# Kernel tuning notes

Hardware: AMD Instinct MI355X
Metric: run time of the kernel (lower is better)

The kernel has to match this reference:

```python
import jax, jax.numpy as jnp
import numpy as np

DIM = 2048          # args.dim
E = 16              # n_routed_experts
TOPK = 2            # n_activated_experts
H = 1408            # moe_inter_dim (expert hidden)
N_SHARED = 2        # n_shared_experts
HS = H * N_SHARED   # shared expert hidden
B, S = 2, 2048
TEMP = 1.0          # gate_temperature


def setup_inputs() -> dict:
    key = jax.random.key(0)
    ks = jax.random.split(key, 8)
    sc = 0.02
    return {
        "x": jax.random.normal(ks[0], (B, S, DIM), dtype=jnp.float32),
        "gate_w": jax.random.normal(ks[1], (E, DIM), dtype=jnp.float32) * sc,
        "w1": jax.random.normal(ks[2], (E, H, DIM), dtype=jnp.float32) * sc,
        "w2": jax.random.normal(ks[3], (E, DIM, H), dtype=jnp.float32) * sc,
        "w3": jax.random.normal(ks[4], (E, H, DIM), dtype=jnp.float32) * sc,
        "sw1": jax.random.normal(ks[5], (HS, DIM), dtype=jnp.float32) * sc,
        "sw2": jax.random.normal(ks[6], (DIM, HS), dtype=jnp.float32) * sc,
        "sw3": jax.random.normal(ks[7], (HS, DIM), dtype=jnp.float32) * sc,
    }


def reference(x, gate_w, w1, w2, w3, sw1, sw2, sw3):
    b, s, d = x.shape
    xf = x.reshape(-1, d)  # [T, D]

    # shared expert (SwiGLU FFN)
    sh = jax.nn.silu(xf @ sw1.T) * (xf @ sw3.T)      # [T, HS]
    shared_out = sh @ sw2.T                           # [T, D]

    # gate (eval mode: no input noise)
    scores = (xf @ gate_w.T) / TEMP                   # [T, E]
    probs = jax.nn.softmax(scores, axis=-1)
    topk_vals, topk_idx = jax.lax.top_k(probs, TOPK)  # sorted desc, matches torch.topk
    topk_vals = topk_vals / (topk_vals.sum(-1, keepdims=True) + 1e-9)

    # combine weights per (token, expert); zero where expert not selected
    w = (jax.nn.one_hot(topk_idx, E, dtype=xf.dtype) * topk_vals[..., None]).sum(1)  # [T, E]

    # all-expert SwiGLU, weighted-combined (w==0 exactly zeroes unselected experts)
    h1 = jnp.einsum('td,ehd->teh', xf, w1)            # [T, E, H]
    h3 = jnp.einsum('td,ehd->teh', xf, w3)
    act = jax.nn.silu(h1) * h3 * w[:, :, None]
    y = jnp.einsum('teh,edh->td', act, w2) + shared_out

    # aux load-balancing loss
    importance = probs.mean(0)                        # [E]
    load = w.sum(0) / (w.sum() + 1e-9)                # [E]
    aux_loss = E * (importance * load).sum()

    return y.reshape(b, s, d), aux_loss
```

## Files before the change

### kernel.cpp

```cpp
#include <hip/hip_runtime.h>
#include <cstdint>

#define TOKS 4096
#define DIMD 2048
#define NE   16
#define HE   1408
#define HSH  2816
#define SLOTS 8192
#define SLOTP 8320
#define MAXTILES 128

typedef unsigned short u16;
typedef __attribute__((ext_vector_type(8))) __bf16 bf16x8;
typedef __attribute__((ext_vector_type(4))) float  f32x4;

__device__ inline unsigned f2bf_pack(float a, float b) {
  unsigned ua = __builtin_bit_cast(unsigned, a);
  unsigned ub = __builtin_bit_cast(unsigned, b);
  ua = (ua + 0x7FFFu + ((ua >> 16) & 1u)) >> 16;
  ub = (ub + 0x7FFFu + ((ub >> 16) & 1u)) >> 16;
  return ua | (ub << 16);
}
__device__ inline u16 f2bf(float a) {
  unsigned ua = __builtin_bit_cast(unsigned, a);
  return (u16)((ua + 0x7FFFu + ((ua >> 16) & 1u)) >> 16);
}
__device__ inline float bf2f(u16 u) {
  return __builtin_bit_cast(float, (unsigned)u << 16);
}
__device__ inline void gload_lds16(const u16* g, u16* l) {
  __builtin_amdgcn_global_load_lds((const __attribute__((address_space(1))) void*)g,
                                   (__attribute__((address_space(3))) void*)l, 16, 0, 0);
}

__global__ __launch_bounds__(64)
void gate2_kernel(const float* __restrict__ x, const float* __restrict__ gw,
                  float* __restrict__ probs, int* __restrict__ sel0, int* __restrict__ sel1,
                  float* __restrict__ wt0, float* __restrict__ wt1)
{
  const int t = blockIdx.x;
  const int l = threadIdx.x;
  const float4* xr = (const float4*)(x + (size_t)t * DIMD);
  float4 xv[8];
#pragma unroll
  for (int j = 0; j < 8; ++j) xv[j] = xr[j * 64 + l];

  float sc[16];
#pragma unroll
  for (int e = 0; e < 16; ++e) {
    const float4* g = (const float4*)(gw + (size_t)e * DIMD);
    float s = 0.f;
#pragma unroll
    for (int j = 0; j < 8; ++j) {
      float4 gv = g[j * 64 + l];
      s += xv[j].x * gv.x + xv[j].y * gv.y + xv[j].z * gv.z + xv[j].w * gv.w;
    }
#pragma unroll
    for (int o = 32; o > 0; o >>= 1) s += __shfl_down(s, o);
    sc[e] = s;
  }
  if (l == 0) {
    float mx = sc[0];
#pragma unroll
    for (int e = 1; e < 16; ++e) mx = fmaxf(mx, sc[e]);
    float pe[16]; float sum = 0.f;
#pragma unroll
    for (int e = 0; e < 16; ++e) { pe[e] = __expf(sc[e] - mx); sum += pe[e]; }
    float inv = 1.f / sum;
    int b0 = -1, b1 = -1; float v0 = -1.f, v1 = -1.f;
#pragma unroll
    for (int e = 0; e < 16; ++e) {
      float p = pe[e] * inv;
      probs[t * 16 + e] = p;
      if (p > v0) { v1 = v0; b1 = b0; v0 = p; b0 = e; }
      else if (p > v1) { v1 = p; b1 = e; }
    }
    float wsum = v0 + v1 + 1e-9f;
    sel0[t] = b0; sel1[t] = b1;
    wt0[t] = v0 / wsum; wt1[t] = v1 / wsum;
  }
}

__global__ __launch_bounds__(256)
void expert_count(const int* __restrict__ sel0, const int* __restrict__ sel1,
                  const float* __restrict__ wt0, const float* __restrict__ wt1,
                  int* __restrict__ counts, float* __restrict__ loadsum)
{
  const int e = blockIdx.x, tid = threadIdx.x;
  int c = 0; float s = 0.f;
  for (int t = tid; t < TOKS; t += 256) {
    if (sel0[t] == e) { c++; s += wt0[t]; }
    else if (sel1[t] == e) { c++; s += wt1[t]; }
  }
  __shared__ int ci[256]; __shared__ float sf[256];
  ci[tid] = c; sf[tid] = s; __syncthreads();
  for (int d = 128; d > 0; d >>= 1) {
    if (tid < d) { ci[tid] += ci[tid + d]; sf[tid] += sf[tid + d]; }
    __syncthreads();
  }
  if (tid == 0) { counts[e] = ci[0]; loadsum[e] = sf[0]; }
}

__global__ __launch_bounds__(256)
void offsets_aux(const float* __restrict__ probs, const int* __restrict__ counts,
                 const float* __restrict__ loadsum, int* __restrict__ offs,
                 int* __restrict__ tile_e, int* __restrict__ tile_m, int* __restrict__ meta,
                 float* __restrict__ out_aux)
{
  const int tid = threadIdx.x;
  float imp[16];
#pragma unroll
  for (int e = 0; e < 16; ++e) imp[e] = 0.f;
  for (int t = tid; t < TOKS; t += 256)
#pragma unroll
    for (int e = 0; e < 16; ++e) imp[e] += probs[t * 16 + e];

  __shared__ float red[256];
  __shared__ float impE[16];
  for (int e = 0; e < 16; ++e) {
    red[tid] = imp[e]; __syncthreads();
    for (int d = 128; d > 0; d >>= 1) {
      if (tid < d) red[tid] += red[tid + d];
      __syncthreads();
    }
    if (tid == 0) impE[e] = red[0];
    __syncthreads();
  }
  if (tid == 0) {
    int off = 0;
    for (int e = 0; e < 16; ++e) { offs[e] = off; off += counts[e]; }
    float tot = 0.f;
    for (int e = 0; e < 16; ++e) tot += loadsum[e];
    float aux = 0.f;
    for (int e = 0; e < 16; ++e) aux += (impE[e] / (float)TOKS) * (loadsum[e] / (tot + 1e-9f));
    *out_aux = 16.f * aux;
    int tile = 0;
    for (int e = 0; e < 16; ++e) {
      int nt = (counts[e] + 127) >> 7;
      for (int k = 0; k < nt; ++k) { tile_e[tile] = e; tile_m[tile] = k << 7; ++tile; }
    }
    meta[0] = tile;
  }
}

__global__ __launch_bounds__(256)
void rank_scatter(const int* __restrict__ sel0, const int* __restrict__ sel1,
                  const float* __restrict__ wt0, const float* __restrict__ wt1,
                  const int* __restrict__ offs, int* __restrict__ toklist2,
                  float* __restrict__ slotwt, int* __restrict__ tokslot)
{
  const int e = blockIdx.x, tid = threadIdx.x;
  const int t0 = tid * 16;
  unsigned flags = 0; int cloc = 0;
#pragma unroll
  for (int j = 0; j < 16; ++j) {
    int t = t0 + j;
    bool f = (sel0[t] == e) || (sel1[t] == e);
    flags |= ((unsigned)f) << j;
    cloc += f;
  }
  __shared__ int psum[256];
  psum[tid] = cloc; __syncthreads();
  for (int d = 1; d < 256; d <<= 1) {
    int v = (tid >= d) ? psum[tid - d] : 0;
    __syncthreads();
    psum[tid] += v;
    __syncthreads();
  }
  int r = offs[e] + psum[tid] - cloc;
  for (int j = 0; j < 16; ++j) {
    if ((flags >> j) & 1u) {
      int t = t0 + j;
      bool first = (sel0[t] == e);
      toklist2[r] = t;
      slotwt[r] = first ? wt0[t] : wt1[t];
      tokslot[2 * t + (first ? 0 : 1)] = r;
      r++;
    }
  }
}

__global__ __launch_bounds__(256)
void cvt_f32_bf16(const float4* __restrict__ src, uint2* __restrict__ dst, int n4)
{
  int i = blockIdx.x * 256 + threadIdx.x;
  int stride = gridDim.x * 256;
  for (; i < n4; i += stride) {
    float4 v = src[i];
    uint2 p; p.x = f2bf_pack(v.x, v.y); p.y = f2bf_pack(v.z, v.w);
    dst[i] = p;
  }
}

__global__ __launch_bounds__(256)
void cvt_expert(const float4* __restrict__ src, uint2* __restrict__ dst,
                int per_e4, int dstride4, int doff4, int total4)
{
  int i = blockIdx.x * 256 + threadIdx.x;
  int stride = gridDim.x * 256;
  for (; i < total4; i += stride) {
    int e = i / per_e4;
    int r = i - e * per_e4;
    float4 v = src[i];
    uint2 p; p.x = f2bf_pack(v.x, v.y); p.y = f2bf_pack(v.z, v.w);
    dst[(size_t)e * dstride4 + doff4 + r] = p;
  }
}

__global__ __launch_bounds__(256)
void gather2(const float* __restrict__ x, const int* __restrict__ toklist2,
             u16* __restrict__ Xg)
{
  int slot = blockIdx.x * 4 + (threadIdx.x >> 6);
  int l = threadIdx.x & 63;
  int tok = toklist2[slot];
  const float4* srcr = (const float4*)(x + (size_t)tok * DIMD);
  uint2* dstr = (uint2*)(Xg + (size_t)slot * DIMD);
#pragma unroll
  for (int j = 0; j < 8; ++j) {
    float4 v = srcr[j * 64 + l];
    uint2 q; q.x = f2bf_pack(v.x, v.y); q.y = f2bf_pack(v.z, v.w);
    dstr[j * 64 + l] = q;
  }
}

template<int MODE>
__global__ __launch_bounds__(256, 3)
void gemm128(const u16* __restrict__ A, const u16* __restrict__ Bg,
             u16* __restrict__ Obf, float* __restrict__ Of,
             const int* __restrict__ counts, const int* __restrict__ offs,
             const int* __restrict__ tile_e, const int* __restrict__ tile_m,
             const int* __restrict__ meta)
{
  constexpr int KD = (MODE == 0) ? DIMD : (MODE == 1) ? HSH : (MODE == 2) ? DIMD : HE;
  constexpr int ND = (MODE == 0) ? 2 * HSH : (MODE == 1) ? DIMD : (MODE == 2) ? HSH : DIMD;

  __shared__ u16 sA[128 * 64];
  __shared__ u16 sB[128 * 64];

  const int tid  = threadIdx.x;
  const int lane = tid & 63;
  const int wave = tid >> 6;
  const int wm = wave >> 1, wn = wave & 1;

  int mbase, nbase;
  int e = 0, cnt = 0, arow0;
  const u16* B = Bg;
  if constexpr (MODE >= 2) {
    int tix = blockIdx.y;
    if (tix >= meta[0]) return;
    e = tile_e[tix];
    cnt = counts[e];
    mbase = tile_m[tix];
    arow0 = offs[e] + mbase;
    nbase = blockIdx.x * 128;
    B = Bg + (size_t)e * ND * KD;
  } else {
    const int nx = gridDim.x;
    int bid = blockIdx.y * nx + blockIdx.x;
    int cpx = (nx * gridDim.y) >> 3;
    int swz = (bid & 7) * cpx + (bid >> 3);
    mbase = (swz / nx) * 128;
    nbase = (swz % nx) * 128;
    arow0 = mbase;
  }

  f32x4 acc[4][4];
#pragma unroll
  for (int i = 0; i < 4; ++i)
#pragma unroll
    for (int j = 0; j < 4; ++j) acc[i][j] = (f32x4){0.f, 0.f, 0.f, 0.f};

  const int srow  = lane >> 3;
  const int sslot = (lane & 7) ^ srow;
  const int scol  = sslot * 8;

  const u16* Bbase = B + (size_t)nbase * KD;

  for (int kb = 0; kb < KD; kb += 64) {
#pragma unroll
    for (int i = 0; i < 4; ++i) {
      int c = wave * 4 + i;
      int row = c * 8 + srow;
      size_t ar;
      if constexpr (MODE >= 2) {
        int rg = arow0 + row;
        if (rg > SLOTS - 1) rg = SLOTS - 1;
        ar = (size_t)rg * KD;
      } else {
        ar = (size_t)(arow0 + row) * KD;
      }
      gload_lds16(A + ar + kb + scol, &sA[c * 512]);
      gload_lds16(Bbase + (size_t)row * KD + kb + scol, &sB[c * 512]);
    }
    __syncthreads();

#pragma unroll
    for (int ks = 0; ks < 2; ++ks) {
      bf16x8 a[4], b[4];
#pragma unroll
      for (int mi = 0; mi < 4; ++mi) {
        int r = wm * 64 + mi * 16 + (lane & 15);
        int s = (ks * 4 + (lane >> 4)) ^ (r & 7);
        a[mi] = *(const bf16x8*)((const char*)sA + r * 128 + s * 16);
      }
#pragma unroll
      for (int ni = 0; ni < 4; ++ni) {
        int r = wn * 64 + ni * 16 + (lane & 15);
        int s = (ks * 4 + (lane >> 4)) ^ (r & 7);
        b[ni] = *(const bf16x8*)((const char*)sB + r * 128 + s * 16);
      }
#pragma unroll
      for (int mi = 0; mi < 4; ++mi)
#pragma unroll
        for (int ni = 0; ni < 4; ++ni)
          acc[mi][ni] = __builtin_amdgcn_mfma_f32_16x16x32_bf16(a[mi], b[ni], acc[mi][ni], 0, 0, 0);
    }
    __syncthreads();
  }

  const int lr4 = (lane >> 4) * 4;
  const int lc  = lane & 15;
#pragma unroll
  for (int mi = 0; mi < 4; ++mi) {
#pragma unroll
    for (int ni = 0; ni < 4; ++ni) {
#pragma unroll
      for (int r = 0; r < 4; ++r) {
        int lrow = wm * 64 + mi * 16 + lr4 + r;
        int col  = nbase + wn * 64 + ni * 16 + lc;
        float v = acc[mi][ni][r];
        if constexpr (MODE == 0) {
          Obf[(size_t)(mbase + lrow) * ND + col] = f2bf(v);
        } else if constexpr (MODE == 1) {
          Of[(size_t)(mbase + lrow) * ND + col] = v;
        } else {
          int grow = mbase + lrow;
          if (grow < cnt) Obf[(size_t)(arow0 + lrow) * ND + col] = f2bf(v);
        }
      }
    }
  }
}

__global__ __launch_bounds__(256)
void combine_sh(const u16* __restrict__ H, u16* __restrict__ U)
{
  int i = blockIdx.x * 256 + threadIdx.x;
  if (i >= TOKS * (HSH / 8)) return;
  int t = i / (HSH / 8);
  int c = (i - t * (HSH / 8)) * 8;
  const u16* h1p = H + (size_t)t * (2 * HSH) + c;
  uint4 va = *(const uint4*)h1p;
  uint4 vb = *(const uint4*)(h1p + HSH);
  const u16* ap = (const u16*)&va;
  const u16* bp = (const u16*)&vb;
  u16 o[8];
#pragma unroll
  for (int j = 0; j < 8; ++j) {
    float v1 = bf2f(ap[j]), v3 = bf2f(bp[j]);
    o[j] = f2bf((v1 / (1.f + __expf(-v1))) * v3);
  }
  *(uint4*)(U + (size_t)t * HSH + c) = *(const uint4*)o;
}

__global__ __launch_bounds__(256)
void combine_r(const u16* __restrict__ H, const float* __restrict__ slotwt,
               u16* __restrict__ Act)
{
  int i = blockIdx.x * 256 + threadIdx.x;
  if (i >= SLOTS * (HE / 8)) return;
  int t = i / (HE / 8);
  int c = (i - t * (HE / 8)) * 8;
  float wt = slotwt[t];
  const u16* h1p = H + (size_t)t * HSH + c;
  uint4 va = *(const uint4*)h1p;
  uint4 vb = *(const uint4*)(h1p + HE);
  const u16* ap = (const u16*)&va;
  const u16* bp = (const u16*)&vb;
  u16 o[8];
#pragma unroll
  for (int j = 0; j < 8; ++j) {
    float v1 = bf2f(ap[j]), v3 = bf2f(bp[j]);
    o[j] = f2bf((v1 / (1.f + __expf(-v1))) * v3 * wt);
  }
  *(uint4*)(Act + (size_t)t * HE + c) = *(const uint4*)o;
}

__global__ __launch_bounds__(256)
void finalize(const u16* __restrict__ Yslot, const int* __restrict__ tokslot,
              float* __restrict__ out)
{
  int i = blockIdx.x * 256 + threadIdx.x;
  int t = i >> 8;
  int c = (i & 255) * 8;
  int s0 = tokslot[2 * t], s1 = tokslot[2 * t + 1];
  uint4 a = *(const uint4*)(Yslot + (size_t)s0 * DIMD + c);
  uint4 b = *(const uint4*)(Yslot + (size_t)s1 * DIMD + c);
  const u16* ap = (const u16*)&a;
  const u16* bp = (const u16*)&b;
  float* op = out + (size_t)t * DIMD + c;
  float4 v0 = *(float4*)op, v1 = *(float4*)(op + 4);
  float vv[8] = {v0.x, v0.y, v0.z, v0.w, v1.x, v1.y, v1.z, v1.w};
#pragma unroll
  for (int j = 0; j < 8; ++j) vv[j] += bf2f(ap[j]) + bf2f(bp[j]);
  *(float4*)op = (float4){vv[0], vv[1], vv[2], vv[3]};
  *(float4*)(op + 4) = (float4){vv[4], vv[5], vv[6], vv[7]};
}

extern "C" void kernel_launch(void* const* d_in, const int* in_sizes, int n_in,
                              void* d_out, int out_size, void* d_ws, size_t ws_size,
                              hipStream_t stream) {
  const float* x      = (const float*)d_in[0];
  const float* gate_w = (const float*)d_in[1];
  const float* w1     = (const float*)d_in[2];
  const float* w2     = (const float*)d_in[3];
  const float* w3     = (const float*)d_in[4];
  const float* sw1    = (const float*)d_in[5];
  const float* sw2    = (const float*)d_in[6];
  const float* sw3    = (const float*)d_in[7];
  float* out = (float*)d_out;

  char* ws = (char*)d_ws;
  size_t o = 0;
  int*   counts   = (int*)(ws + o);   o += 256;
  int*   offsv    = (int*)(ws + o);   o += 256;
  float* loadsum  = (float*)(ws + o); o += 256;
  int*   tile_e   = (int*)(ws + o);   o += MAXTILES * 4;
  int*   tile_m   = (int*)(ws + o);   o += MAXTILES * 4;
  int*   meta     = (int*)(ws + o);   o += 256;
  int*   sel0     = (int*)(ws + o);   o += TOKS * 4;
  int*   sel1     = (int*)(ws + o);   o += TOKS * 4;
  float* wt0      = (float*)(ws + o); o += TOKS * 4;
  float* wt1      = (float*)(ws + o); o += TOKS * 4;
  int*   tokslot  = (int*)(ws + o);   o += TOKS * 2 * 4;
  int*   toklist2 = (int*)(ws + o);   o += SLOTS * 4;
  float* slotwt   = (float*)(ws + o); o += SLOTS * 4;
  float* probs    = (float*)(ws + o); o += TOKS * 16 * 4;

  o = 1 << 20;
  u16* xbf   = (u16*)(ws + o); o += (size_t)TOKS * DIMD * 2;
  u16* Xg    = (u16*)(ws + o); o += (size_t)SLOTP * DIMD * 2;
  u16* w13b  = (u16*)(ws + o); o += (size_t)NE * HSH * DIMD * 2;
  u16* w2b   = (u16*)(ws + o); o += (size_t)NE * DIMD * HE * 2;
  u16* sw13b = (u16*)(ws + o); o += (size_t)(2 * HSH) * DIMD * 2;
  u16* sw2b  = (u16*)(ws + o); o += (size_t)DIMD * HSH * 2;
  u16* H     = (u16*)(ws + o); o += (size_t)SLOTP * HSH * 2;
  u16* UA    = (u16*)(ws + o); o += (size_t)SLOTP * HE * 2;
  u16* Yslot = Xg;

  gate2_kernel<<<TOKS, 64, 0, stream>>>(x, gate_w, probs, sel0, sel1, wt0, wt1);
  expert_count<<<NE, 256, 0, stream>>>(sel0, sel1, wt0, wt1, counts, loadsum);
  offsets_aux<<<1, 256, 0, stream>>>(probs, counts, loadsum, offsv, tile_e, tile_m, meta,
                                     out + (size_t)TOKS * DIMD);
  rank_scatter<<<NE, 256, 0, stream>>>(sel0, sel1, wt0, wt1, offsv, toklist2, slotwt, tokslot);

  cvt_f32_bf16<<<2048, 256, 0, stream>>>((const float4*)x, (uint2*)xbf, TOKS * DIMD / 4);
  cvt_f32_bf16<<<1024, 256, 0, stream>>>((const float4*)sw1, (uint2*)sw13b, HSH * DIMD / 4);
  cvt_f32_bf16<<<1024, 256, 0, stream>>>((const float4*)sw3, (uint2*)sw13b + HSH * DIMD / 4, HSH * DIMD / 4);
  cvt_f32_bf16<<<1024, 256, 0, stream>>>((const float4*)sw2, (uint2*)sw2b, DIMD * HSH / 4);
  cvt_f32_bf16<<<4096, 256, 0, stream>>>((const float4*)w2, (uint2*)w2b, NE * DIMD * HE / 4);
  cvt_expert<<<4096, 256, 0, stream>>>((const float4*)w1, (uint2*)w13b,
                                       HE * DIMD / 4, HSH * DIMD / 4, 0, NE * HE * DIMD / 4);
  cvt_expert<<<4096, 256, 0, stream>>>((const float4*)w3, (uint2*)w13b,
                                       HE * DIMD / 4, HSH * DIMD / 4, HE * DIMD / 4, NE * HE * DIMD / 4);
  gather2<<<SLOTS / 4, 256, 0, stream>>>(x, toklist2, Xg);

  gemm128<0><<<dim3(2 * HSH / 128, TOKS / 128), 256, 0, stream>>>(
      xbf, sw13b, H, nullptr, nullptr, nullptr, nullptr, nullptr, nullptr);
  combine_sh<<<TOKS * (HSH / 8) / 256, 256, 0, stream>>>(H, UA);
  gemm128<1><<<dim3(DIMD / 128, TOKS / 128), 256, 0, stream>>>(
      UA, sw2b, nullptr, out, nullptr, nullptr, nullptr, nullptr, nullptr);

  gemm128<2><<<dim3(HSH / 128, 80), 256, 0, stream>>>(
      Xg, w13b, H, nullptr, counts, offsv, tile_e, tile_m, meta);
  combine_r<<<SLOTS * (HE / 8) / 256, 256, 0, stream>>>(H, slotwt, UA);
  gemm128<3><<<dim3(DIMD / 128, 80), 256, 0, stream>>>(
      UA, w2b, Yslot, nullptr, counts, offsv, tile_e, tile_m, meta);
  finalize<<<TOKS * DIMD / 8 / 256, 256, 0, stream>>>(Yslot, tokslot, out);
}
```

Measured before the change: 770.2 us.

## Use 256-wide double-buffered GEMM tiles with 512 threads and XCD-aware swizzle

```diff
diff --git a/kernel.cpp b/kernel.cpp
--- a/kernel.cpp
+++ b/kernel.cpp
@@ -136,8 +136,8 @@
     *out_aux = 16.f * aux;
     int tile = 0;
     for (int e = 0; e < 16; ++e) {
-      int nt = (counts[e] + 127) >> 7;
-      for (int k = 0; k < nt; ++k) { tile_e[tile] = e; tile_m[tile] = k << 7; ++tile; }
+      int nt = (counts[e] + 255) >> 8;
+      for (int k = 0; k < nt; ++k) { tile_e[tile] = e; tile_m[tile] = k << 8; ++tile; }
     }
     meta[0] = tile;
   }
@@ -224,9 +224,9 @@
   }
 }
 
-template<int MODE>
-__global__ __launch_bounds__(256, 3)
-void gemm128(const u16* __restrict__ A, const u16* __restrict__ Bg,
+template<int MODE, int BMT>
+__global__ __launch_bounds__(512, 2)
+void gemm256(const u16* __restrict__ A, const u16* __restrict__ Bg,
              u16* __restrict__ Obf, float* __restrict__ Of,
              const int* __restrict__ counts, const int* __restrict__ offs,
              const int* __restrict__ tile_e, const int* __restrict__ tile_m,
@@ -234,14 +234,17 @@
 {
   constexpr int KD = (MODE == 0) ? DIMD : (MODE == 1) ? HSH : (MODE == 2) ? DIMD : HE;
   constexpr int ND = (MODE == 0) ? 2 * HSH : (MODE == 1) ? DIMD : (MODE == 2) ? HSH : DIMD;
-
-  __shared__ u16 sA[128 * 64];
-  __shared__ u16 sB[128 * 64];
+  constexpr int BM = BMT * 32;
+  constexpr int NT = KD / 64;
+
+  __shared__ u16 sA[2][BM * 64];
+  __shared__ u16 sB[2][256 * 64];
 
   const int tid  = threadIdx.x;
   const int lane = tid & 63;
   const int wave = tid >> 6;
-  const int wm = wave >> 1, wn = wave & 1;
+  const int wm = wave >> 2;
+  const int wn = wave & 3;
 
   int mbase, nbase;
   int e = 0, cnt = 0, arow0;
@@ -253,82 +256,114 @@
     cnt = counts[e];
     mbase = tile_m[tix];
     arow0 = offs[e] + mbase;
-    nbase = blockIdx.x * 128;
+    nbase = blockIdx.x * 256;
     B = Bg + (size_t)e * ND * KD;
   } else {
     const int nx = gridDim.x;
+    int nwg = nx * gridDim.y;
     int bid = blockIdx.y * nx + blockIdx.x;
-    int cpx = (nx * gridDim.y) >> 3;
-    int swz = (bid & 7) * cpx + (bid >> 3);
-    mbase = (swz / nx) * 128;
-    nbase = (swz % nx) * 128;
+    int q = nwg >> 3, r2 = nwg & 7;
+    int xcd = bid & 7, pos = bid >> 3;
+    int wgid = (xcd < r2 ? xcd * (q + 1) : r2 * (q + 1) + (xcd - r2) * q) + pos;
+    mbase = (wgid / nx) * BM;
+    nbase = (wgid % nx) * 256;
     arow0 = mbase;
   }
 
-  f32x4 acc[4][4];
-#pragma unroll
-  for (int i = 0; i < 4; ++i)
+  f32x4 acc[BMT][4];
+#pragma unroll
+  for (int i = 0; i < BMT; ++i)
 #pragma unroll
     for (int j = 0; j < 4; ++j) acc[i][j] = (f32x4){0.f, 0.f, 0.f, 0.f};
 
-  const int srow  = lane >> 3;
-  const int sslot = (lane & 7) ^ srow;
-  const int scol  = sslot * 8;
-
+  const int srow = lane >> 3;
+  const int scol = ((lane & 7) ^ srow) * 8;
   const u16* Bbase = B + (size_t)nbase * KD;
 
-  for (int kb = 0; kb < KD; kb += 64) {
-#pragma unroll
-    for (int i = 0; i < 4; ++i) {
-      int c = wave * 4 + i;
-      int row = c * 8 + srow;
-      size_t ar;
-      if constexpr (MODE >= 2) {
-        int rg = arow0 + row;
-        if (rg > SLOTS - 1) rg = SLOTS - 1;
-        ar = (size_t)rg * KD;
-      } else {
-        ar = (size_t)(arow0 + row) * KD;
+  const u16* Asrc[BMT / 2];
+#pragma unroll
+  for (int i = 0; i < BMT / 2; ++i) {
+    int c = wave * (BMT / 2) + i;
+    int row = c * 8 + srow;
+    int rg = arow0 + row;
+    if constexpr (MODE >= 2) { if (rg > SLOTS - 1) rg = SLOTS - 1; }
+    Asrc[i] = A + (size_t)rg * KD + scol;
+  }
+  const u16* Bsrc[4];
+#pragma unroll
+  for (int i = 0; i < 4; ++i) {
+    int c = wave * 4 + i;
+    Bsrc[i] = Bbase + (size_t)(c * 8 + srow) * KD + scol;
+  }
+
+#define STAGE_T(bb, kb) do {                                                    \
+    _Pragma("unroll") for (int i_ = 0; i_ < BMT / 2; ++i_)                      \
+      gload_lds16(Asrc[i_] + (kb), &sA[bb][(wave * (BMT / 2) + i_) * 512]);     \
+    _Pragma("unroll") for (int i_ = 0; i_ < 4; ++i_)                            \
+      gload_lds16(Bsrc[i_] + (kb), &sB[bb][(wave * 4 + i_) * 512]);             \
+  } while (0)
+
+  const int lm = lane & 15, hi = lane >> 4;
+  int aoff0[BMT], boff0[4];
+#pragma unroll
+  for (int mi = 0; mi < BMT; ++mi) {
+    int r = wm * (BMT * 16) + mi * 16 + lm;
+    aoff0[mi] = r * 128 + ((hi ^ (r & 7)) << 4);
+  }
+#pragma unroll
+  for (int ni = 0; ni < 4; ++ni) {
+    int r = wn * 64 + ni * 16 + lm;
+    boff0[ni] = r * 128 + ((hi ^ (r & 7)) << 4);
+  }
+
+  STAGE_T(0, 0);
+  STAGE_T(1, 64);
+  int cur = 0;
+  for (int t = 0; t < NT; ++t) {
+    if (t < NT - 1) {
+      if constexpr (BMT == 8) asm volatile("s_waitcnt vmcnt(8)" ::: "memory");
+      else                    asm volatile("s_waitcnt vmcnt(6)" ::: "memory");
+    } else {
+      asm volatile("s_waitcnt vmcnt(0)" ::: "memory");
+    }
+    __builtin_amdgcn_s_barrier();
+    __builtin_amdgcn_sched_barrier(0);
+
+    const char* sAc = (const char*)&sA[cur][0];
+    const char* sBc = (const char*)&sB[cur][0];
+    __builtin_amdgcn_s_setprio(1);
+#pragma unroll
+    for (int ks = 0; ks < 2; ++ks) {
+      const int kx = ks << 6;
+      bf16x8 b[4];
+#pragma unroll
+      for (int ni = 0; ni < 4; ++ni) b[ni] = *(const bf16x8*)(sBc + (boff0[ni] ^ kx));
+#pragma unroll
+      for (int mi = 0; mi < BMT; ++mi) {
+        bf16x8 av = *(const bf16x8*)(sAc + (aoff0[mi] ^ kx));
+#pragma unroll
+        for (int ni = 0; ni < 4; ++ni)
+          acc[mi][ni] = __builtin_amdgcn_mfma_f32_16x16x32_bf16(av, b[ni], acc[mi][ni], 0, 0, 0);
       }
-      gload_lds16(A + ar + kb + scol, &sA[c * 512]);
-      gload_lds16(Bbase + (size_t)row * KD + kb + scol, &sB[c * 512]);
-    }
-    __syncthreads();
-
-#pragma unroll
-    for (int ks = 0; ks < 2; ++ks) {
-      bf16x8 a[4], b[4];
-#pragma unroll
-      for (int mi = 0; mi < 4; ++mi) {
-        int r = wm * 64 + mi * 16 + (lane & 15);
-        int s = (ks * 4 + (lane >> 4)) ^ (r & 7);
-        a[mi] = *(const bf16x8*)((const char*)sA + r * 128 + s * 16);
-      }
-#pragma unroll
-      for (int ni = 0; ni < 4; ++ni) {
-        int r = wn * 64 + ni * 16 + (lane & 15);
-        int s = (ks * 4 + (lane >> 4)) ^ (r & 7);
-        b[ni] = *(const bf16x8*)((const char*)sB + r * 128 + s * 16);
-      }
-#pragma unroll
-      for (int mi = 0; mi < 4; ++mi)
-#pragma unroll
-        for (int ni = 0; ni < 4; ++ni)
-          acc[mi][ni] = __builtin_amdgcn_mfma_f32_16x16x32_bf16(a[mi], b[ni], acc[mi][ni], 0, 0, 0);
-    }
-    __syncthreads();
-  }
-
-  const int lr4 = (lane >> 4) * 4;
-  const int lc  = lane & 15;
-#pragma unroll
-  for (int mi = 0; mi < 4; ++mi) {
+    }
+    __builtin_amdgcn_s_setprio(0);
+    __builtin_amdgcn_sched_barrier(0);
+    __builtin_amdgcn_s_barrier();
+    __builtin_amdgcn_sched_barrier(0);
+    if (t + 2 < NT) STAGE_T(cur, (t + 2) * 64);
+    cur ^= 1;
+  }
+#undef STAGE_T
+
+  const int lr4 = hi * 4;
+#pragma unroll
+  for (int mi = 0; mi < BMT; ++mi) {
 #pragma unroll
     for (int ni = 0; ni < 4; ++ni) {
 #pragma unroll
       for (int r = 0; r < 4; ++r) {
-        int lrow = wm * 64 + mi * 16 + lr4 + r;
-        int col  = nbase + wn * 64 + ni * 16 + lc;
+        int lrow = wm * (BMT * 16) + mi * 16 + lr4 + r;
+        int col  = nbase + wn * 64 + ni * 16 + lm;
         float v = acc[mi][ni][r];
         if constexpr (MODE == 0) {
           Obf[(size_t)(mbase + lrow) * ND + col] = f2bf(v);
@@ -466,16 +501,16 @@
                                        HE * DIMD / 4, HSH * DIMD / 4, HE * DIMD / 4, NE * HE * DIMD / 4);
   gather2<<<SLOTS / 4, 256, 0, stream>>>(x, toklist2, Xg);
 
-  gemm128<0><<<dim3(2 * HSH / 128, TOKS / 128), 256, 0, stream>>>(
+  gemm256<0, 8><<<dim3(2 * HSH / 256, TOKS / 256), 512, 0, stream>>>(
       xbf, sw13b, H, nullptr, nullptr, nullptr, nullptr, nullptr, nullptr);
   combine_sh<<<TOKS * (HSH / 8) / 256, 256, 0, stream>>>(H, UA);
-  gemm128<1><<<dim3(DIMD / 128, TOKS / 128), 256, 0, stream>>>(
+  gemm256<1, 4><<<dim3(DIMD / 256, TOKS / 128), 512, 0, stream>>>(
       UA, sw2b, nullptr, out, nullptr, nullptr, nullptr, nullptr, nullptr);
 
-  gemm128<2><<<dim3(HSH / 128, 80), 256, 0, stream>>>(
+  gemm256<2, 8><<<dim3(HSH / 256, 48), 512, 0, stream>>>(
       Xg, w13b, H, nullptr, counts, offsv, tile_e, tile_m, meta);
   combine_r<<<SLOTS * (HE / 8) / 256, 256, 0, stream>>>(H, slotwt, UA);
-  gemm128<3><<<dim3(DIMD / 128, 80), 256, 0, stream>>>(
+  gemm256<3, 8><<<dim3(DIMD / 256, 48), 512, 0, stream>>>(
       UA, w2b, Yslot, nullptr, counts, offsv, tile_e, tile_m, meta);
   finalize<<<TOKS * DIMD / 8 / 256, 256, 0, stream>>>(Yslot, tokslot, out);
 }
```

Result: slower. 841.6 us (+9.3%).
